# Kernel optimization log

Hardware: AMD Instinct MI355X
Metric: run time of the kernel (lower is better)

Reference implementation:

```python
import jax, jax.numpy as jnp
import numpy as np

N_NODES = 100000

def _gcn_conv(x, W, b, src, dst, n_nodes):
    # PyG GCNConv: h = x @ W; add self-loops; deg over dst; norm = d^-1/2[src]*d^-1/2[dst];
    # out = scatter_add(norm * h[src] -> dst) + b
    h = x @ W  # [N, out]
    deg = jax.ops.segment_sum(jnp.ones_like(dst, dtype=x.dtype), dst, num_segments=n_nodes)
    dinv = jnp.where(deg > 0, jax.lax.rsqrt(deg), 0.0)
    norm = dinv[src] * dinv[dst]  # [E]
    msg = h[src] * norm[:, None]  # [E, out]
    out = jax.ops.segment_sum(msg, dst, num_segments=n_nodes)
    return out + b

def setup_inputs() -> dict:
    key = jax.random.key(0)
    k1, k2, k3, k4 = jax.random.split(key, 4)
    x = jax.random.normal(k1, (N_NODES, 165), dtype=jnp.float32)
    edge_index = jax.random.randint(k2, (2, 1600000), 0, N_NODES, dtype=jnp.int64)
    # glorot-ish init for weights
    W1 = jax.random.normal(k3, (165, 128), dtype=jnp.float32) * (1.0 / np.sqrt(165))
    b1 = jnp.zeros((128,), dtype=jnp.float32)
    W4 = jax.random.normal(k4, (128, 1), dtype=jnp.float32) * (1.0 / np.sqrt(128))
    b4 = jnp.zeros((1,), dtype=jnp.float32)
    return {"x": x, "edge_index": edge_index, "W1": W1, "b1": b1, "W4": W4, "b4": b4}

def reference(x, edge_index, W1, b1, W4, b4):
    n = x.shape[0]
    loop = jnp.arange(n, dtype=edge_index.dtype)
    src = jnp.concatenate([edge_index[0], loop])  # add self-loops
    dst = jnp.concatenate([edge_index[1], loop])
    h = _gcn_conv(x, W1, b1, src, dst, n)
    h = jax.nn.relu(h)
    # dropout p=0.1 is identity at inference (training=False)
    out = _gcn_conv(h, W4, b4, src, dst, n)
    return jax.nn.sigmoid(out)
```

## Files before the change

kernel.cpp:

```cpp
#include <hip/hip_runtime.h>
#include <math.h>

#define N_NODES 100000

using bf16x8 = __attribute__((ext_vector_type(8))) short;
using f32x4  = __attribute__((ext_vector_type(4))) float;

static inline size_t align_up(size_t x, size_t a){ return (x + a - 1) & ~(a - 1); }

__device__ __forceinline__ unsigned short f2bf(float f){
  unsigned u = __float_as_uint(f);
  u = (u + 0x7fffu + ((u >> 16) & 1u)) >> 16;
  return (unsigned short)u;
}
__device__ __forceinline__ float bf2f(unsigned short h){
  return __uint_as_float(((unsigned)h) << 16);
}
__device__ __forceinline__ float bf_lo(unsigned u){ return __uint_as_float(u << 16); }
__device__ __forceinline__ float bf_hi(unsigned u){ return __uint_as_float(u & 0xffff0000u); }

__global__ void k_zero(int* __restrict__ p, int n){
  int i = blockIdx.x*blockDim.x + threadIdx.x;
  if(i < n) p[i] = 0;
}

__global__ void k_convert_count(const int* __restrict__ ei,
                                int* __restrict__ src32, int* __restrict__ dst32,
                                int* __restrict__ rank, int* __restrict__ cnt_p, int E){
  __shared__ int s_is64;
  if(threadIdx.x == 0){
    int is64 = 1;
    for(int k=0;k<64;k++){ if(ei[2*k+1] != 0){ is64 = 0; break; } }
    s_is64 = is64;
  }
  __syncthreads();
  int is64 = s_is64;
  int stride = gridDim.x * blockDim.x;
  for(int e = blockIdx.x*blockDim.x + threadIdx.x; e < E; e += stride){
    int s, d;
    if(is64){ s = ei[2*e]; d = ei[2*(E + e)]; }
    else    { s = ei[e];   d = ei[E + e]; }
    src32[e] = s; dst32[e] = d;
    rank[e] = atomicAdd(&cnt_p[(size_t)d*16], 1);
  }
}

__global__ void k_scan_part(const int* __restrict__ cnt_p, int* __restrict__ bsum, int n){
  __shared__ int red[256];
  int b = blockIdx.x, t = threadIdx.x;
  int base = b*1024 + t*4;
  int s = 0;
  #pragma unroll
  for(int k=0;k<4;k++){ int i = base + k; if(i < n) s += cnt_p[(size_t)i*16]; }
  red[t] = s; __syncthreads();
  for(int off=128; off>0; off>>=1){
    if(t < off) red[t] += red[t+off];
    __syncthreads();
  }
  if(t==0) bsum[b] = red[0];
}

__global__ void k_scan_top(int* __restrict__ bsum, int nb){
  __shared__ int sh[128];
  int t = threadIdx.x;
  int v = (t < nb) ? bsum[t] : 0;
  sh[t] = v; __syncthreads();
  int inc = v;
  for(int off=1; off<128; off<<=1){
    int add = (t >= off) ? sh[t-off] : 0;
    __syncthreads();
    inc += add; sh[t] = inc;
    __syncthreads();
  }
  if(t < nb) bsum[t] = inc - v;
}

__global__ void k_scan_down(const int* __restrict__ cnt_p, const int* __restrict__ bsum,
                            int* __restrict__ offs, float* __restrict__ dinv, int n, int E){
  __shared__ int sh[256];
  int b = blockIdx.x, t = threadIdx.x;
  int base = b*1024 + t*4;
  int c[4]; int local = 0;
  #pragma unroll
  for(int k=0;k<4;k++){ int i = base + k; c[k] = (i < n) ? cnt_p[(size_t)i*16] : 0; local += c[k]; }
  sh[t] = local; __syncthreads();
  int inc = local;
  for(int off=1; off<256; off<<=1){
    int add = (t >= off) ? sh[t-off] : 0;
    __syncthreads();
    inc += add; sh[t] = inc;
    __syncthreads();
  }
  int running = bsum[b] + (inc - local);
  #pragma unroll
  for(int k=0;k<4;k++){
    int i = base + k;
    if(i < n){
      offs[i] = running;
      dinv[i] = rsqrtf((float)(c[k] + 1));
      running += c[k];
    }
  }
  if(b==0 && t==0) offs[n] = E;
}

__global__ void k_fill(const int* __restrict__ src32, const int* __restrict__ dst32,
                       const int* __restrict__ rank, const int* __restrict__ offs,
                       int* __restrict__ csr, int E){
  int stride = gridDim.x * blockDim.x;
  for(int e = blockIdx.x*blockDim.x + threadIdx.x; e < E; e += stride){
    csr[offs[dst32[e]] + rank[e]] = src32[e];
  }
}

__global__ void k_prep_w1(const float* __restrict__ w1, unsigned short* __restrict__ w1b){
  int id = blockIdx.x*blockDim.x + threadIdx.x;
  if(id >= 6*8*64) return;
  int lane = id & 63;
  int st = id >> 6;
  int s = st >> 3, t = st & 7;
  int g = lane >> 4;
  int nn = t*16 + (lane & 15);
  unsigned short* dst = w1b + (size_t)((s*8 + t)*64 + lane)*16;
  #pragma unroll
  for(int j=0;j<8;j++){
    int k = s*32 + g*8 + j;
    float v = (k < 165) ? w1[(size_t)k*128 + nn] : 0.f;
    unsigned short hi = f2bf(v);
    unsigned short lo = f2bf(v - bf2f(hi));
    dst[j] = hi; dst[8+j] = lo;
  }
}

__global__ __launch_bounds__(256) void k_gemm_mfma(const float* __restrict__ x,
                                                   const unsigned short* __restrict__ w1b,
                                                   const float* __restrict__ dinv,
                                                   unsigned short* __restrict__ hsc, int n){
  int lane = threadIdx.x & 63;
  int w    = threadIdx.x >> 6;
  int m    = lane & 15;
  int g    = lane >> 4;
  int row  = blockIdx.x*64 + w*16 + m;
  int rowc = row < n ? row : n-1;
  const float* xr = x + (size_t)rowc * 165;
  const bf16x8* wb = (const bf16x8*)w1b;

  f32x4 acc[8];
  #pragma unroll
  for(int t=0;t<8;t++){ acc[t][0]=0.f; acc[t][1]=0.f; acc[t][2]=0.f; acc[t][3]=0.f; }

  #pragma unroll
  for(int s=0;s<6;s++){
    int k0 = s*32 + g*8;
    float v[8];
    if(s < 5){
      #pragma unroll
      for(int j=0;j<8;j++) v[j] = xr[k0+j];
    }else{
      #pragma unroll
      for(int j=0;j<8;j++){ int k = k0+j; v[j] = (k < 165) ? xr[k] : 0.f; }
    }
    bf16x8 ah, al;
    #pragma unroll
    for(int j=0;j<8;j++){
      unsigned short hi = f2bf(v[j]);
      ah[j] = (short)hi;
      al[j] = (short)f2bf(v[j] - bf2f(hi));
    }
    #pragma unroll
    for(int t=0;t<8;t++){
      int bidx = ((s*8 + t)*64 + lane)*2;
      bf16x8 bh = wb[bidx];
      bf16x8 bl = wb[bidx + 1];
      acc[t] = __builtin_amdgcn_mfma_f32_16x16x32_bf16(bh, ah, acc[t], 0, 0, 0);
      acc[t] = __builtin_amdgcn_mfma_f32_16x16x32_bf16(bh, al, acc[t], 0, 0, 0);
      acc[t] = __builtin_amdgcn_mfma_f32_16x16x32_bf16(bl, ah, acc[t], 0, 0, 0);
    }
  }

  if(row < n){
    float di = dinv[row];
    unsigned* hp = (unsigned*)(hsc + (size_t)row*128);
    #pragma unroll
    for(int t=0;t<8;t++){
      unsigned short q0 = f2bf(acc[t][0]*di);
      unsigned short q1 = f2bf(acc[t][1]*di);
      unsigned short q2 = f2bf(acc[t][2]*di);
      unsigned short q3 = f2bf(acc[t][3]*di);
      int nbase = t*16 + g*4;
      hp[(nbase>>1)    ] = (unsigned)q0 | ((unsigned)q1 << 16);
      hp[(nbase>>1) + 1] = (unsigned)q2 | ((unsigned)q3 << 16);
    }
  }
}

__global__ __launch_bounds__(256) void k_agg1(const unsigned short* __restrict__ hsc,
                                              const int* __restrict__ offs,
                                              const int* __restrict__ csr,
                                              const float* __restrict__ dinv,
                                              const float* __restrict__ b1,
                                              const float* __restrict__ w4,
                                              float* __restrict__ g, int n){
  int wv = threadIdx.x >> 6;
  int lane = threadIdx.x & 63;
  int i = blockIdx.x * 4 + wv;
  if(i >= n) return;

  float di = dinv[i];
  int s0 = offs[i], s1 = offs[i+1];
  int f = lane * 2;

  float ax = 0.f, ay = 0.f;
  int e = s0;
  for(; e + 1 < s1; e += 2){
    int sA = csr[e], sB = csr[e+1];
    unsigned uA = ((const unsigned*)(hsc + (size_t)sA*128))[lane];
    unsigned uB = ((const unsigned*)(hsc + (size_t)sB*128))[lane];
    ax += bf_lo(uA) + bf_lo(uB);
    ay += bf_hi(uA) + bf_hi(uB);
  }
  if(e < s1){
    unsigned uA = ((const unsigned*)(hsc + (size_t)csr[e]*128))[lane];
    ax += bf_lo(uA);
    ay += bf_hi(uA);
  }
  unsigned uS = ((const unsigned*)(hsc + (size_t)i*128))[lane];
  ax = di * (ax + bf_lo(uS));
  ay = di * (ay + bf_hi(uS));

  float2 bb = *(const float2*)&b1[f];
  float o0 = fmaxf(ax + bb.x, 0.f);
  float o1 = fmaxf(ay + bb.y, 0.f);

  float2 wv4 = *(const float2*)&w4[f];
  float p = o0*wv4.x + o1*wv4.y;
  #pragma unroll
  for(int offm=32; offm>0; offm>>=1) p += __shfl_xor(p, offm, 64);
  if(lane == 0) g[i] = di * p;
}

__global__ void k_agg2c(const float* __restrict__ g, const int* __restrict__ offs,
                        const int* __restrict__ csr, const float* __restrict__ dinv,
                        const float* __restrict__ b4, float* __restrict__ out, int n){
  int lane = threadIdx.x & 63;
  int wv   = threadIdx.x >> 6;
  int sub  = lane & 7;
  int i = blockIdx.x*32 + wv*8 + (lane >> 3);
  if(i >= n) return;
  int s1 = offs[i+1];
  float p = 0.f;
  for(int e = offs[i] + sub; e < s1; e += 8) p += g[csr[e]];
  p += __shfl_xor(p, 4, 8);
  p += __shfl_xor(p, 2, 8);
  p += __shfl_xor(p, 1, 8);
  if(sub == 0){
    float di = dinv[i];
    float z = di*(p + g[i]) + b4[0];
    out[i] = 1.f/(1.f+expf(-z));
  }
}

extern "C" void kernel_launch(void* const* d_in, const int* in_sizes, int n_in,
                              void* d_out, int out_size, void* d_ws, size_t ws_size,
                              hipStream_t stream){
  const float* x  = (const float*)d_in[0];
  const int*   ei = (const int*)d_in[1];
  const float* w1 = (const float*)d_in[2];
  const float* b1 = (const float*)d_in[3];
  const float* w4 = (const float*)d_in[4];
  const float* b4 = (const float*)d_in[5];
  float* out = (float*)d_out;

  const int n = N_NODES;
  const int E = in_sizes[1] / 2;

  char* ws = (char*)d_ws;
  size_t off = 0;
  auto carve = [&](size_t bytes)->void*{
    void* p = ws + off; off = align_up(off + bytes, 256); return p;
  };
  int*   cnt_p = (int*)carve((size_t)n*16*4);
  int*   offs  = (int*)carve((size_t)(n+1)*4);
  int*   bsum  = (int*)carve(128*4);
  float* dinv  = (float*)carve((size_t)n*4);
  int*   src32 = (int*)carve((size_t)E*4);
  int*   dst32 = (int*)carve((size_t)E*4);
  int*   rank  = (int*)carve((size_t)E*4);
  int*   csr   = (int*)carve((size_t)E*4);
  unsigned short* w1b = (unsigned short*)carve((size_t)6*8*64*16*2);
  unsigned short* hsc = (unsigned short*)carve((size_t)n*128*2);
  float* g     = (float*)carve((size_t)n*4);
  (void)ws_size;

  int nb = (n + 1023) / 1024;

  k_zero         <<<(n*16+255)/256, 256, 0, stream>>>(cnt_p, n*16);
  k_convert_count<<<2048, 256, 0, stream>>>(ei, src32, dst32, rank, cnt_p, E);
  k_scan_part    <<<nb, 256, 0, stream>>>(cnt_p, bsum, n);
  k_scan_top     <<<1, 128, 0, stream>>>(bsum, nb);
  k_scan_down    <<<nb, 256, 0, stream>>>(cnt_p, bsum, offs, dinv, n, E);
  k_fill         <<<2048, 256, 0, stream>>>(src32, dst32, rank, offs, csr, E);
  k_prep_w1      <<<12, 256, 0, stream>>>(w1, w1b);
  k_gemm_mfma    <<<(n+63)/64, 256, 0, stream>>>(x, w1b, dinv, hsc, n);
  k_agg1         <<<(n+3)/4, 256, 0, stream>>>(hsc, offs, csr, dinv, b1, w4, g, n);
  k_agg2c        <<<(n+31)/32, 256, 0, stream>>>(g, offs, csr, dinv, b4, out, n);
}
```

Measured before the change: 380.5 us.

## Stage x tile in LDS for GEMM and split edges across half-waves in aggregation

The GEMM kernel now loads each block's 64 rows of x into shared memory with a coalesced flat copy, padded to a stride of 172. The MFMA loop then reads from LDS instead of doing strided per-lane global loads. The aggregation kernel splits each node's edge list between the two half-waves, with each lane loading 8 bytes (4 bf16 features), and combines the halves with a cross-half shuffle. The intent is better memory coalescing and more gather parallelism, at the cost of about 44KB of LDS per block (which may reduce occupancy) and an extra shuffle reduction.

```diff
diff --git a/kernel.cpp b/kernel.cpp
--- a/kernel.cpp
+++ b/kernel.cpp
@@ -136,18 +136,30 @@
                                                    const unsigned short* __restrict__ w1b,
                                                    const float* __restrict__ dinv,
                                                    unsigned short* __restrict__ hsc, int n){
+  __shared__ float xs[64*172];
+  int t = threadIdx.x;
+  int rowbase = blockIdx.x*64;
+  int nrow = min(64, n - rowbase);
+  int nfl = nrow * 165;
+  const float* xblk = x + (size_t)rowbase*165;
+  for(int f = t; f < nfl; f += 256){
+    int r = f / 165;
+    int c = f - r*165;
+    xs[r*172 + c] = xblk[f];
+  }
+  __syncthreads();
+
   int lane = threadIdx.x & 63;
   int w    = threadIdx.x >> 6;
   int m    = lane & 15;
   int g    = lane >> 4;
-  int row  = blockIdx.x*64 + w*16 + m;
-  int rowc = row < n ? row : n-1;
-  const float* xr = x + (size_t)rowc * 165;
+  int row  = rowbase + w*16 + m;
+  const float* xr = xs + (w*16 + m)*172;
   const bf16x8* wb = (const bf16x8*)w1b;
 
   f32x4 acc[8];
   #pragma unroll
-  for(int t=0;t<8;t++){ acc[t][0]=0.f; acc[t][1]=0.f; acc[t][2]=0.f; acc[t][3]=0.f; }
+  for(int q=0;q<8;q++){ acc[q][0]=0.f; acc[q][1]=0.f; acc[q][2]=0.f; acc[q][3]=0.f; }
 
   #pragma unroll
   for(int s=0;s<6;s++){
@@ -168,13 +180,13 @@
       al[j] = (short)f2bf(v[j] - bf2f(hi));
     }
     #pragma unroll
-    for(int t=0;t<8;t++){
-      int bidx = ((s*8 + t)*64 + lane)*2;
+    for(int q=0;q<8;q++){
+      int bidx = ((s*8 + q)*64 + lane)*2;
       bf16x8 bh = wb[bidx];
       bf16x8 bl = wb[bidx + 1];
-      acc[t] = __builtin_amdgcn_mfma_f32_16x16x32_bf16(bh, ah, acc[t], 0, 0, 0);
-      acc[t] = __builtin_amdgcn_mfma_f32_16x16x32_bf16(bh, al, acc[t], 0, 0, 0);
-      acc[t] = __builtin_amdgcn_mfma_f32_16x16x32_bf16(bl, ah, acc[t], 0, 0, 0);
+      acc[q] = __builtin_amdgcn_mfma_f32_16x16x32_bf16(bh, ah, acc[q], 0, 0, 0);
+      acc[q] = __builtin_amdgcn_mfma_f32_16x16x32_bf16(bh, al, acc[q], 0, 0, 0);
+      acc[q] = __builtin_amdgcn_mfma_f32_16x16x32_bf16(bl, ah, acc[q], 0, 0, 0);
     }
   }
 
@@ -182,12 +194,12 @@
     float di = dinv[row];
     unsigned* hp = (unsigned*)(hsc + (size_t)row*128);
     #pragma unroll
-    for(int t=0;t<8;t++){
-      unsigned short q0 = f2bf(acc[t][0]*di);
-      unsigned short q1 = f2bf(acc[t][1]*di);
-      unsigned short q2 = f2bf(acc[t][2]*di);
-      unsigned short q3 = f2bf(acc[t][3]*di);
-      int nbase = t*16 + g*4;
+    for(int q=0;q<8;q++){
+      unsigned short q0 = f2bf(acc[q][0]*di);
+      unsigned short q1 = f2bf(acc[q][1]*di);
+      unsigned short q2 = f2bf(acc[q][2]*di);
+      unsigned short q3 = f2bf(acc[q][3]*di);
+      int nbase = q*16 + g*4;
       hp[(nbase>>1)    ] = (unsigned)q0 | ((unsigned)q1 << 16);
       hp[(nbase>>1) + 1] = (unsigned)q2 | ((unsigned)q3 << 16);
     }
@@ -203,39 +215,52 @@
                                               float* __restrict__ g, int n){
   int wv = threadIdx.x >> 6;
   int lane = threadIdx.x & 63;
+  int half = lane >> 5;
+  int sub  = lane & 31;
   int i = blockIdx.x * 4 + wv;
   if(i >= n) return;
 
   float di = dinv[i];
   int s0 = offs[i], s1 = offs[i+1];
-  int f = lane * 2;
-
-  float ax = 0.f, ay = 0.f;
-  int e = s0;
-  for(; e + 1 < s1; e += 2){
-    int sA = csr[e], sB = csr[e+1];
-    unsigned uA = ((const unsigned*)(hsc + (size_t)sA*128))[lane];
-    unsigned uB = ((const unsigned*)(hsc + (size_t)sB*128))[lane];
-    ax += bf_lo(uA) + bf_lo(uB);
-    ay += bf_hi(uA) + bf_hi(uB);
+  const unsigned* base = (const unsigned*)hsc;
+
+  float a0=0.f, a1=0.f, a2=0.f, a3=0.f;
+  int e = s0 + half;
+  for(; e + 2 < s1; e += 4){
+    int sA = csr[e], sB = csr[e+2];
+    uint2 uA = *(const uint2*)(base + (size_t)sA*64 + sub*2);
+    uint2 uB = *(const uint2*)(base + (size_t)sB*64 + sub*2);
+    a0 += bf_lo(uA.x) + bf_lo(uB.x);
+    a1 += bf_hi(uA.x) + bf_hi(uB.x);
+    a2 += bf_lo(uA.y) + bf_lo(uB.y);
+    a3 += bf_hi(uA.y) + bf_hi(uB.y);
   }
   if(e < s1){
-    unsigned uA = ((const unsigned*)(hsc + (size_t)csr[e]*128))[lane];
-    ax += bf_lo(uA);
-    ay += bf_hi(uA);
-  }
-  unsigned uS = ((const unsigned*)(hsc + (size_t)i*128))[lane];
-  ax = di * (ax + bf_lo(uS));
-  ay = di * (ay + bf_hi(uS));
-
-  float2 bb = *(const float2*)&b1[f];
-  float o0 = fmaxf(ax + bb.x, 0.f);
-  float o1 = fmaxf(ay + bb.y, 0.f);
-
-  float2 wv4 = *(const float2*)&w4[f];
-  float p = o0*wv4.x + o1*wv4.y;
-  #pragma unroll
-  for(int offm=32; offm>0; offm>>=1) p += __shfl_xor(p, offm, 64);
+    int sA = csr[e];
+    uint2 uA = *(const uint2*)(base + (size_t)sA*64 + sub*2);
+    a0 += bf_lo(uA.x); a1 += bf_hi(uA.x);
+    a2 += bf_lo(uA.y); a3 += bf_hi(uA.y);
+  }
+  if(half == 0){
+    uint2 uS = *(const uint2*)(base + (size_t)i*64 + sub*2);
+    a0 += bf_lo(uS.x); a1 += bf_hi(uS.x);
+    a2 += bf_lo(uS.y); a3 += bf_hi(uS.y);
+  }
+  a0 += __shfl_xor(a0, 32, 64);
+  a1 += __shfl_xor(a1, 32, 64);
+  a2 += __shfl_xor(a2, 32, 64);
+  a3 += __shfl_xor(a3, 32, 64);
+
+  int f = sub*4;
+  float4 bb  = *(const float4*)&b1[f];
+  float4 wv4 = *(const float4*)&w4[f];
+  float o0 = fmaxf(di*a0 + bb.x, 0.f);
+  float o1 = fmaxf(di*a1 + bb.y, 0.f);
+  float o2 = fmaxf(di*a2 + bb.z, 0.f);
+  float o3 = fmaxf(di*a3 + bb.w, 0.f);
+  float p = o0*wv4.x + o1*wv4.y + o2*wv4.z + o3*wv4.w;
+  #pragma unroll
+  for(int offm=16; offm>0; offm>>=1) p += __shfl_xor(p, offm, 64);
   if(lane == 0) g[i] = di * p;
 }
 
```

After: 350.9 us. 7.8% less time.
